# Kernel tuning notes

Measured on AMD Instinct MI355X. Metric: run time of the kernel, lower is better.

The kernel has to match this reference:

```python
import jax, jax.numpy as jnp
import numpy as np

NUM_CLASSES = 80
NUM_ATTRIB = 85
SCORE_THR = 0.05
CONF_THR = 0.005
IOU_THR = 0.45
MAX_DET = 100
PRE_NMS_TOPK = 4096  # top-k pre-filter; greedy NMS over these candidates


def _make_anchors():
    strides = [32, 16, 8]
    base_sizes = [[(116, 90), (156, 198), (373, 326)],
                  [(30, 61), (62, 45), (59, 119)],
                  [(10, 13), (16, 30), (33, 23)]]
    feat_sizes = [(19, 19), (38, 38), (76, 76)]
    anchors, strs = [], []
    for s, bs, (fh, fw) in zip(strides, base_sizes, feat_sizes):
        c = s / 2.0
        base = np.array([[c - 0.5 * w, c - 0.5 * h, c + 0.5 * w, c + 0.5 * h]
                         for (w, h) in bs], np.float32)
        xx = np.tile(np.arange(fw, dtype=np.float32) * s, fh)
        yy = np.repeat(np.arange(fh, dtype=np.float32) * s, fw)
        shifts = np.stack([xx, yy, xx, yy], -1)  # [HW,4]
        a = (shifts[:, None, :] + base[None, :, :]).reshape(-1, 4)  # location-major, anchor-minor
        anchors.append(a)
        strs.append(np.full(a.shape[0], s, np.float32))
    return np.concatenate(anchors), np.concatenate(strs)

_ANCHORS, _STRIDES = _make_anchors()


def _iou_one_to_many(box, boxes):
    tl = jnp.maximum(box[:2], boxes[:, :2])
    br = jnp.minimum(box[2:], boxes[:, 2:])
    inter = jnp.prod(jnp.clip(br - tl, 0.0), axis=-1)
    a1 = jnp.prod(box[2:] - box[:2])
    a2 = jnp.prod(boxes[:, 2:] - boxes[:, :2], axis=-1)
    return inter / (a1 + a2 - inter + 1e-12)


def _per_image(pred):  # pred: [N, 85]
    anchors = jnp.asarray(_ANCHORS)
    strides = jnp.asarray(_STRIDES)
    xy = jax.nn.sigmoid(pred[:, :2])
    obj = jax.nn.sigmoid(pred[:, 4])
    cls = jax.nn.sigmoid(pred[:, 5:])
    # decode_bboxes
    centers = (anchors[:, :2] + anchors[:, 2:]) * 0.5 + (xy - 0.5) * strides[:, None]
    whs = (anchors[:, 2:] - anchors[:, :2]) * 0.5 * jnp.exp(pred[:, 2:4])
    boxes = jnp.concatenate([centers - whs, centers + whs], axis=-1)  # [N,4]
    # conf threshold on objectness + score threshold on raw class score (torch order),
    # then multiply by objectness score factor
    valid = (obj[:, None] >= CONF_THR) & (cls > SCORE_THR)
    scores = jnp.where(valid, cls * obj[:, None], -jnp.inf).reshape(-1)  # [N*C]
    top_s, top_i = jax.lax.top_k(scores, PRE_NMS_TOPK)
    bidx = top_i // NUM_CLASSES
    labels = (top_i % NUM_CLASSES).astype(jnp.int32)
    cboxes = boxes[bidx]  # [K,4]
    finite = jnp.isfinite(top_s)
    max_coord = jnp.max(jnp.where(finite[:, None], cboxes, 0.0))
    off = labels.astype(boxes.dtype) * (max_coord + 1.0)  # per-class offset trick
    nms_boxes = cboxes + off[:, None]

    def body(i, state):
        alive, dets, det_labels = state
        j = jnp.argmax(alive)
        s = alive[j]
        keep = s > 0.0
        det = jnp.where(keep, jnp.concatenate([cboxes[j], s[None]]), 0.0)
        dets = dets.at[i].set(det)
        det_labels = det_labels.at[i].set(jnp.where(keep, labels[j], -1))
        suppress = _iou_one_to_many(nms_boxes[j], nms_boxes) > IOU_THR
        alive = jnp.where(suppress, -jnp.inf, alive).at[j].set(-jnp.inf)
        return alive, dets, det_labels

    dets0 = jnp.zeros((MAX_DET, 5), boxes.dtype)
    lbl0 = jnp.full((MAX_DET,), -1, jnp.int32)
    _, dets, det_labels = jax.lax.fori_loop(0, MAX_DET, body, (top_s, dets0, lbl0))
    return dets, det_labels


def _forward(pred_maps):
    B = pred_maps[0].shape[0]
    flat = [p.transpose(0, 2, 3, 1).reshape(B, -1, NUM_ATTRIB) for p in pred_maps]
    preds = jnp.concatenate(flat, axis=1)  # [B, N, 85]
    return jax.vmap(_per_image)(preds)  # dets [B,100,5], labels [B,100]


def setup_inputs() -> dict:
    key = jax.random.key(0)
    k0, k1, k2 = jax.random.split(key, 3)
    return {
        "pred_map0": jax.random.normal(k0, (16, 255, 19, 19), jnp.float32),
        "pred_map1": jax.random.normal(k1, (16, 255, 38, 38), jnp.float32),
        "pred_map2": jax.random.normal(k2, (16, 255, 76, 76), jnp.float32),
    }


def reference(pred_map0, pred_map1, pred_map2):
    return _forward([pred_map0, pred_map1, pred_map2])
```

## Files before the change

kernel.cpp:

```cpp
#include <hip/hip_runtime.h>
#include <stdint.h>
#include <math.h>

typedef unsigned long long u64;

#define CONF_THR   0.005f
#define SCORE_THRf 0.05f
#define IOU_THR    0.45f
#define TOPK       4096
#define MAXDET     100
#define NHIST      8192
#define NIMG       16
#define BCAP       8192
#define NSLICE     27
#define NBLK       (NIMG * NSLICE)
#define LCAP       1024

__constant__ float c_half[3][3][2] = {
  {{58.0f, 45.0f}, {78.0f, 99.0f}, {186.5f, 163.0f}},
  {{15.0f, 30.5f}, {31.0f, 22.5f}, {29.5f, 59.5f}},
  {{5.0f, 6.5f},  {8.0f, 15.0f},  {16.5f, 11.5f}},
};

__device__ __forceinline__ float sigmoidf_(float x) {
  return 1.0f / (1.0f + expf(-x));
}

__device__ __forceinline__ bool slice4_decode(const float* __restrict__ p0,
                                              const float* __restrict__ p1,
                                              const float* __restrict__ p2,
                                              int bx, int tid,
                                              int& b, const float*& q, int& HW,
                                              int& nstart, int& a, int& hw0, int& mi) {
  b = bx / NSLICE;
  int r = bx % NSLICE;
  int h0;
  if (r < 18)      { mi = 2; a = r / 6;         h0 = (r % 6) * 1024; }
  else if (r < 24) { mi = 1; a = (r - 18) >> 1; h0 = ((r - 18) & 1) * 1024; }
  else             { mi = 0; a = r - 24;        h0 = 0; }
  const float* p;
  if (mi == 2)      { p = p2; HW = 5776; nstart = 5415; }
  else if (mi == 1) { p = p1; HW = 1444; nstart = 1083; }
  else              { p = p0; HW = 361;  nstart = 0; }
  hw0 = h0 + tid * 4;
  if (hw0 >= HW) return false;
  q = p + (size_t)b * 255 * HW;
  return true;
}

template <bool PRIV>
__global__ void __launch_bounds__(256) k_hist(const float* __restrict__ p0,
                                              const float* __restrict__ p1,
                                              const float* __restrict__ p2,
                                              unsigned* __restrict__ outHist) {
  __shared__ unsigned lh[NHIST];
  for (int i = threadIdx.x; i < NHIST; i += 256) lh[i] = 0;
  __syncthreads();
  int b; const float* q; int HW, nstart, a, hw0, mi;
  bool act = slice4_decode(p0, p1, p2, blockIdx.x, threadIdx.x, b, q, HW, nstart, a, hw0, mi);
  if (act) {
    const float* orow = q + (size_t)(a * 85 + 4) * HW;
    float so[4]; bool ov[4] = {false, false, false, false};
    if (mi != 0) {
      float4 o = *(const float4*)(orow + hw0);
      so[0] = sigmoidf_(o.x); so[1] = sigmoidf_(o.y);
      so[2] = sigmoidf_(o.z); so[3] = sigmoidf_(o.w);
      #pragma unroll
      for (int k = 0; k < 4; ++k) ov[k] = so[k] >= CONF_THR;
    } else {
      #pragma unroll
      for (int k = 0; k < 4; ++k)
        if (hw0 + k < HW) { so[k] = sigmoidf_(orow[hw0 + k]); ov[k] = so[k] >= CONF_THR; }
    }
    for (int c = 0; c < 80; ++c) {
      const float* crow = q + (size_t)(a * 85 + 5 + c) * HW;
      float cv[4];
      if (mi != 0) {
        float4 v = *(const float4*)(crow + hw0);
        cv[0] = v.x; cv[1] = v.y; cv[2] = v.z; cv[3] = v.w;
      } else {
        #pragma unroll
        for (int k = 0; k < 4; ++k) cv[k] = (hw0 + k < HW) ? crow[hw0 + k] : -100.0f;
      }
      #pragma unroll
      for (int k = 0; k < 4; ++k) {
        if (!ov[k]) continue;
        float cs = sigmoidf_(cv[k]);
        if (cs > SCORE_THRf)
          atomicAdd(&lh[__float_as_uint(__fmul_rn(cs, so[k])) >> 17], 1u);
      }
    }
  }
  __syncthreads();
  if (PRIV) {
    unsigned* dst = outHist + (size_t)blockIdx.x * NHIST;
    for (int i = threadIdx.x * 4; i < NHIST; i += 1024)
      *(uint4*)(dst + i) = *(const uint4*)(&lh[i]);
  } else {
    unsigned* dst = outHist + (size_t)(blockIdx.x / NSLICE) * NHIST;
    for (int i = threadIdx.x; i < NHIST; i += 256) if (lh[i]) atomicAdd(&dst[i], lh[i]);
  }
}

__global__ void __launch_bounds__(256) k_merge(const unsigned* __restrict__ priv,
                                               unsigned* __restrict__ merged) {
  const int b = blockIdx.y;
  const int u = blockIdx.x * 256 + threadIdx.x;
  const unsigned* base = priv + (size_t)b * NSLICE * NHIST + u;
  unsigned s = 0;
  #pragma unroll
  for (int sl = 0; sl < NSLICE; ++sl) s += base[(size_t)sl * NHIST];
  merged[(size_t)b * NHIST + u] = s;
}

__global__ void k_scan(const unsigned* __restrict__ hist, int* __restrict__ bb1) {
  __shared__ unsigned h[NHIST];
  __shared__ unsigned csum[256];
  const int b = blockIdx.x;
  const unsigned* gh = hist + (size_t)b * NHIST;
  for (int i = threadIdx.x; i < NHIST; i += 256) h[i] = gh[i];
  __syncthreads();
  unsigned s = 0;
  for (int j = 0; j < 32; ++j) s += h[threadIdx.x * 32 + j];
  csum[threadIdx.x] = s;
  __syncthreads();
  if (threadIdx.x == 0) {
    unsigned acc = 0; int found = -1;
    for (int c2 = 255; c2 >= 0; --c2) {
      if (acc + csum[c2] >= TOPK) {
        for (int k2 = c2 * 32 + 31; k2 >= c2 * 32; --k2) {
          if (acc + h[k2] >= TOPK) { found = k2; break; }
          acc += h[k2];
        }
        break;
      } else acc += csum[c2];
    }
    bb1[b] = found;
  }
}

__global__ void __launch_bounds__(256) k_collect(const float* __restrict__ p0,
                                                 const float* __restrict__ p1,
                                                 const float* __restrict__ p2,
                                                 const int* __restrict__ bb1v,
                                                 unsigned* __restrict__ candCount,
                                                 unsigned* __restrict__ bCount,
                                                 u64* __restrict__ candKeys,
                                                 u64* __restrict__ blist) {
  __shared__ u64 wbuf[LCAP];
  __shared__ u64 bbuf[LCAP];
  __shared__ unsigned cnt2[2];
  __shared__ unsigned base2[2];
  if (threadIdx.x < 2) cnt2[threadIdx.x] = 0;
  __syncthreads();
  int b; const float* q; int HW, nstart, a, hw0, mi;
  bool act = slice4_decode(p0, p1, p2, blockIdx.x, threadIdx.x, b, q, HW, nstart, a, hw0, mi);
  const int bglobal = blockIdx.x / NSLICE;
  const int Bb1 = bb1v[bglobal];
  u64* ckg = candKeys + (size_t)bglobal * TOPK;
  u64* blg = blist + (size_t)bglobal * BCAP;

  if (act) {
    const float T = (Bb1 > 0) ? __uint_as_float((unsigned)Bb1 << 17) : 0.0f;
    const float* orow = q + (size_t)(a * 85 + 4) * HW;
    float so[4]; bool ov[4] = {false, false, false, false};
    if (mi != 0) {
      float4 o = *(const float4*)(orow + hw0);
      so[0] = sigmoidf_(o.x); so[1] = sigmoidf_(o.y);
      so[2] = sigmoidf_(o.z); so[3] = sigmoidf_(o.w);
      #pragma unroll
      for (int k = 0; k < 4; ++k) ov[k] = so[k] >= CONF_THR;
    } else {
      #pragma unroll
      for (int k = 0; k < 4; ++k)
        if (hw0 + k < HW) { so[k] = sigmoidf_(orow[hw0 + k]); ov[k] = so[k] >= CONF_THR; }
    }
    float cth[4];
    #pragma unroll
    for (int k = 0; k < 4; ++k) {
      cth[k] = 1e30f;
      if (ov[k]) {
        cth[k] = -1e30f;
        if (Bb1 > 0) {
          float u = __fdiv_rn(T, so[k]);
          cth[k] = (u >= 1.0f) ? 15.0f : (logf(__fdiv_rn(u, __fsub_rn(1.0f, u))) - 0.05f);
        }
      }
    }
    for (int c = 0; c < 80; ++c) {
      const float* crow = q + (size_t)(a * 85 + 5 + c) * HW;
      float cv[4];
      if (mi != 0) {
        float4 v = *(const float4*)(crow + hw0);
        cv[0] = v.x; cv[1] = v.y; cv[2] = v.z; cv[3] = v.w;
      } else {
        #pragma unroll
        for (int k = 0; k < 4; ++k) cv[k] = (hw0 + k < HW) ? crow[hw0 + k] : -100.0f;
      }
      #pragma unroll
      for (int k = 0; k < 4; ++k) {
        if (cv[k] <= cth[k]) continue;
        float cs = sigmoidf_(cv[k]);
        if (cs <= SCORE_THRf) continue;
        unsigned bits = __float_as_uint(__fmul_rn(cs, so[k]));
        int bkt = (int)(bits >> 17);
        if (bkt < Bb1) continue;
        unsigned idx = (unsigned)((nstart + (hw0 + k) * 3 + a) * 80 + c);
        u64 key = ((u64)(bits ^ 0x80000000u) << 32) | (u64)(0xFFFFFFFFu - idx);
        if (bkt > Bb1) {
          unsigned pos = atomicAdd(&cnt2[0], 1u);
          if (pos < LCAP) wbuf[pos] = key;
          else { unsigned g = atomicAdd(&candCount[bglobal], 1u); if (g < TOPK) ckg[g] = key; }
        } else {
          unsigned pos = atomicAdd(&cnt2[1], 1u);
          if (pos < LCAP) bbuf[pos] = key;
          else { unsigned g = atomicAdd(&bCount[bglobal], 1u); if (g < BCAP) blg[g] = key; }
        }
      }
    }
  }
  __syncthreads();
  unsigned wn = min(cnt2[0], (unsigned)LCAP);
  unsigned bn = min(cnt2[1], (unsigned)LCAP);
  if (threadIdx.x == 0) base2[0] = wn ? atomicAdd(&candCount[bglobal], wn) : 0u;
  if (threadIdx.x == 1) base2[1] = bn ? atomicAdd(&bCount[bglobal], bn) : 0u;
  __syncthreads();
  for (unsigned i = threadIdx.x; i < wn; i += 256) {
    unsigned g = base2[0] + i; if (g < TOPK) ckg[g] = wbuf[i];
  }
  for (unsigned i = threadIdx.x; i < bn; i += 256) {
    unsigned g = base2[1] + i; if (g < BCAP) blg[g] = bbuf[i];
  }
}

__device__ __forceinline__ int swz(int i) { return i ^ ((i >> 4) & 0xF); }

__device__ __forceinline__ u64 shflx64(u64 x, int m) {
  unsigned lo = __shfl_xor((unsigned)x, m);
  unsigned hi = __shfl_xor((unsigned)(x >> 32), m);
  return ((u64)hi << 32) | lo;
}

template <int V>
__device__ void bitonic_hybrid_desc(u64* sb, u64 (&r)[V], int t) {
  const int N = 1024 * V;
  for (int k = 2; k <= N; k <<= 1) {
    for (int j = k >> 1; j > 0; j >>= 1) {
      if (j >= 64 * V) {
        __syncthreads();
        #pragma unroll
        for (int v = 0; v < V; ++v) sb[swz(t * V + v)] = r[v];
        __syncthreads();
        #pragma unroll
        for (int v = 0; v < V; ++v) {
          int i = t * V + v;
          u64 A = r[v], B = sb[swz(i ^ j)];
          bool up = (i & k) == 0, lower = (i & j) == 0;
          r[v] = (up == lower) ? (A > B ? A : B) : (A < B ? A : B);
        }
      } else if (j >= V) {
        int d = j / V;
        #pragma unroll
        for (int v = 0; v < V; ++v) {
          int i = t * V + v;
          u64 A = r[v], B = shflx64(r[v], d);
          bool up = (i & k) == 0, lower = (i & j) == 0;
          r[v] = (up == lower) ? (A > B ? A : B) : (A < B ? A : B);
        }
      } else {
        #pragma unroll
        for (int v = 0; v < V; ++v) {
          if ((v & j) == 0) {
            int i = t * V + v;
            u64 A = r[v], B = r[v ^ j];
            bool up = (i & k) == 0;
            u64 mx = A > B ? A : B, mn = A > B ? B : A;
            r[v] = up ? mx : mn; r[v ^ j] = up ? mn : mx;
          }
        }
      }
    }
  }
}

__global__ void __launch_bounds__(1024) k_sortdecode(
    const unsigned* __restrict__ candCount, const unsigned* __restrict__ bCount,
    u64* __restrict__ candKeys, const u64* __restrict__ blist,
    const float* __restrict__ p0, const float* __restrict__ p1, const float* __restrict__ p2,
    float4* __restrict__ boxS, float* __restrict__ maxcv) {
  __shared__ u64 sb[8192];
  const int b = blockIdx.x, t = threadIdx.x;
  unsigned C1 = candCount[b]; if (C1 > TOPK) C1 = TOPK;
  unsigned m = bCount[b];     if (m > BCAP) m = BCAP;
  int need = TOPK - (int)C1;
  int take = need > 0 ? (need < (int)m ? need : (int)m) : 0;
  const u64* bl = blist + (size_t)b * BCAP;
  u64* ck = candKeys + (size_t)b * TOPK;
  if (take > 0) {
    u64 r8[8];
    #pragma unroll
    for (int v = 0; v < 8; ++v) { int i = t * 8 + v; r8[v] = (i < (int)m) ? bl[i] : 0ull; }
    bitonic_hybrid_desc<8>(sb, r8, t);
    __syncthreads();
    #pragma unroll
    for (int v = 0; v < 8; ++v) sb[swz(t * 8 + v)] = r8[v];
  }
  __syncthreads();
  u64 r4[4];
  #pragma unroll
  for (int v = 0; v < 4; ++v) {
    int i = t * 4 + v;
    u64 key = 0ull;
    if (i < (int)C1) key = ck[i];
    else if (i < (int)C1 + take) key = sb[swz(i - (int)C1)];
    r4[v] = key;
  }
  __syncthreads();
  bitonic_hybrid_desc<4>(sb, r4, t);
  float lmax = -INFINITY;
  float4* bs = boxS + (size_t)b * TOPK;
  #pragma unroll
  for (int v = 0; v < 4; ++v) {
    int i = t * 4 + v;
    u64 key = r4[v];
    ck[i] = key;
    float4 bx = make_float4(0.f, 0.f, 0.f, 0.f);
    float contrib = 0.0f;
    if (key != 0ull) {
      unsigned idx = 0xFFFFFFFFu - (unsigned)(key & 0xFFFFFFFFull);
      int n = (int)(idx / 80u);
      const float* p; int HW, W, nstart, L; float fs;
      if (n < 1083)      { p = p0; HW = 361;  W = 19; nstart = 0;    fs = 32.f; L = 0; }
      else if (n < 5415) { p = p1; HW = 1444; W = 38; nstart = 1083; fs = 16.f; L = 1; }
      else               { p = p2; HW = 5776; W = 76; nstart = 5415; fs = 8.f;  L = 2; }
      int r = n - nstart; int hw = r / 3; int an = r % 3;
      int gx = hw % W;    int gy = hw / W;
      const float* qq = p + (size_t)b * 255 * HW + hw;
      float tx = qq[(size_t)(an * 85 + 0) * HW];
      float ty = qq[(size_t)(an * 85 + 1) * HW];
      float tw = qq[(size_t)(an * 85 + 2) * HW];
      float th = qq[(size_t)(an * 85 + 3) * HW];
      float acx = __fadd_rn((float)gx * fs, 0.5f * fs);
      float acy = __fadd_rn((float)gy * fs, 0.5f * fs);
      float sx = sigmoidf_(tx), sy = sigmoidf_(ty);
      float cx = __fadd_rn(acx, __fmul_rn(__fsub_rn(sx, 0.5f), fs));
      float cy = __fadd_rn(acy, __fmul_rn(__fsub_rn(sy, 0.5f), fs));
      float wx = __fmul_rn(c_half[L][an][0], expf(tw));
      float wy = __fmul_rn(c_half[L][an][1], expf(th));
      bx.x = __fsub_rn(cx, wx); bx.y = __fsub_rn(cy, wy);
      bx.z = __fadd_rn(cx, wx); bx.w = __fadd_rn(cy, wy);
      contrib = fmaxf(fmaxf(bx.x, bx.y), fmaxf(bx.z, bx.w));
    }
    bs[i] = bx;
    lmax = fmaxf(lmax, contrib);
  }
  float* red = (float*)(sb + 4096);
  red[t] = lmax;
  for (int s = 512; s > 0; s >>= 1) {
    __syncthreads();
    if (t < s) red[t] = fmaxf(red[t], red[t + s]);
  }
  __syncthreads();
  if (t == 0) maxcv[b] = red[0];
}

__global__ void __launch_bounds__(64) k_nms(const u64* __restrict__ candKeys,
                                            const float4* __restrict__ boxS,
                                            const float* __restrict__ maxcv,
                                            float* __restrict__ out) {
  const int b = blockIdx.x;
  const int lane = threadIdx.x;
  float* dets = out + (size_t)b * (MAXDET * 5);
  float* lbls = out + (size_t)NIMG * MAXDET * 5 + (size_t)b * MAXDET;
  for (int i = lane; i < MAXDET; i += 64) {
    dets[i * 5 + 0] = 0.f; dets[i * 5 + 1] = 0.f; dets[i * 5 + 2] = 0.f;
    dets[i * 5 + 3] = 0.f; dets[i * 5 + 4] = 0.f;
    lbls[i] = -1.0f;
  }
  const float mc1 = __fadd_rn(maxcv[b], 1.0f);
  const u64* ck = candKeys + (size_t)b * TOPK;
  const float4* bs = boxS + (size_t)b * TOPK;
  float pbx1[2], pby1[2], pbx2[2], pby2[2], parea[2];
  int P = 0;
  bool done = false;
  for (int base = 0; base < TOPK && !done; base += 64) {
    const int e = base + lane;
    u64 key = ck[e];
    float score = -INFINITY; int c = 0;
    float4 bx = bs[e];
    if (key) {
      unsigned mb = (unsigned)(key >> 32);
      score = __uint_as_float(mb ^ 0x80000000u);
      unsigned idx = 0xFFFFFFFFu - (unsigned)(key & 0xFFFFFFFFull);
      c = (int)(idx % 80u);
    }
    float off = __fmul_rn((float)c, mc1);
    float nx1 = __fadd_rn(bx.x, off), ny1 = __fadd_rn(bx.y, off);
    float nx2 = __fadd_rn(bx.z, off), ny2 = __fadd_rn(bx.w, off);
    for (int tt = 0; tt < 64; ++tt) {
      float s_e = __shfl(score, tt);
      if (!(s_e > 0.0f)) { done = true; break; }
      float ex1 = __shfl(nx1, tt), ey1 = __shfl(ny1, tt);
      float ex2 = __shfl(nx2, tt), ey2 = __shfl(ny2, tt);
      float ea = __fmul_rn(__fsub_rn(ex2, ex1), __fsub_rn(ey2, ey1));
      bool sup = false;
      #pragma unroll
      for (int k2 = 0; k2 < 2; ++k2) {
        int pi = k2 * 64 + lane;
        if (pi < P) {
          float tlx = fmaxf(pbx1[k2], ex1), tly = fmaxf(pby1[k2], ey1);
          float brx = fminf(pbx2[k2], ex2), bry = fminf(pby2[k2], ey2);
          float iw = fmaxf(__fsub_rn(brx, tlx), 0.0f);
          float ih = fmaxf(__fsub_rn(bry, tly), 0.0f);
          float inter = __fmul_rn(iw, ih);
          float denom = __fadd_rn(__fsub_rn(__fadd_rn(parea[k2], ea), inter), 1e-12f);
          float iou = __fdiv_rn(inter, denom);
          if (iou > IOU_THR) sup = true;
        }
      }
      if (!__any(sup)) {
        float cx1 = __shfl(bx.x, tt), cy1 = __shfl(bx.y, tt);
        float cx2 = __shfl(bx.z, tt), cy2 = __shfl(bx.w, tt);
        int   ce  = __shfl(c, tt);
        if (lane == (P & 63)) {
          int slot = P >> 6;
          pbx1[slot] = ex1; pby1[slot] = ey1; pbx2[slot] = ex2; pby2[slot] = ey2;
          parea[slot] = ea;
        }
        if (lane == 0) {
          dets[P * 5 + 0] = cx1; dets[P * 5 + 1] = cy1;
          dets[P * 5 + 2] = cx2; dets[P * 5 + 3] = cy2;
          dets[P * 5 + 4] = s_e;
          lbls[P] = (float)ce;
        }
        ++P;
        if (P == MAXDET) { done = true; break; }
      }
    }
  }
}

extern "C" void kernel_launch(void* const* d_in, const int* in_sizes, int n_in,
                              void* d_out, int out_size, void* d_ws, size_t ws_size,
                              hipStream_t stream) {
  const float* p0 = (const float*)d_in[0];
  const float* p1 = (const float*)d_in[1];
  const float* p2 = (const float*)d_in[2];
  float* out = (float*)d_out;
  char* ws = (char*)d_ws;

  const size_t OFF_MERGED = 0;
  const size_t OFF_CNT    = 524288;
  const size_t OFF_CK     = 524544;
  const size_t OFF_BL     = 1048832;
  const size_t OFF_BOX    = 2097408;
  const size_t OFF_PRIV   = 3145984;
  const size_t NEED_PRIV  = OFF_PRIV + (size_t)NBLK * NHIST * 4;

  unsigned* merged = (unsigned*)(ws + OFF_MERGED);
  unsigned* candCount = (unsigned*)(ws + OFF_CNT);
  unsigned* bCount = candCount + 16;
  int* bb1 = (int*)(bCount + 16);
  float* maxcv = (float*)(bb1 + 16);
  u64* candKeys = (u64*)(ws + OFF_CK);
  u64* blist = (u64*)(ws + OFF_BL);
  float4* boxS = (float4*)(ws + OFF_BOX);
  unsigned* priv = (unsigned*)(ws + OFF_PRIV);

  const bool use_priv = ws_size >= NEED_PRIV;
  if (use_priv) {
    hipMemsetAsync(ws + OFF_CNT, 0, 256, stream);
    k_hist<true><<<NBLK, 256, 0, stream>>>(p0, p1, p2, priv);
    k_merge<<<dim3(NHIST / 256, NIMG), 256, 0, stream>>>(priv, merged);
  } else {
    hipMemsetAsync(ws, 0, OFF_CNT + 256, stream);
    k_hist<false><<<NBLK, 256, 0, stream>>>(p0, p1, p2, merged);
  }
  k_scan<<<NIMG, 256, 0, stream>>>(merged, bb1);
  k_collect<<<NBLK, 256, 0, stream>>>(p0, p1, p2, bb1, candCount, bCount, candKeys, blist);
  k_sortdecode<<<NIMG, 1024, 0, stream>>>(candCount, bCount, candKeys, blist,
                                          p0, p1, p2, boxS, maxcv);
  k_nms<<<NIMG, 64, 0, stream>>>(candKeys, boxS, maxcv, out);
}
```

Measured before the change: 461.2 us.

## Split sort into boundary-select, per-chunk sorts, and merge; finer histogram slicing

The single per-image sort+decode kernel (16 blocks) is split into three kernels. A boundary-bucket select sorts only the needed boundary candidates, 64 blocks each sort a 1024-key chunk with the correct bitonic direction offset, and a final kernel runs only the last two merge stages before decoding boxes. The histogram kernel also moves to 48 slices of 128 threads per image to raise block-level parallelism over the input reads. The cost is extra kernel launches and global round-trips of the candidate keys, plus a plain LDS bitonic sort for the boundary list.

```diff
diff --git a/kernel.cpp b/kernel.cpp
--- a/kernel.cpp
+++ b/kernel.cpp
@@ -12,9 +12,11 @@
 #define NHIST      8192
 #define NIMG       16
 #define BCAP       8192
-#define NSLICE     27
-#define NBLK       (NIMG * NSLICE)
 #define LCAP       1024
+#define NSLICE_C   27
+#define NBLK_C     (NIMG * NSLICE_C)
+#define NSLICE_H   48
+#define NBLK_H     (NIMG * NSLICE_H)
 
 __constant__ float c_half[3][3][2] = {
   {{58.0f, 45.0f}, {78.0f, 99.0f}, {186.5f, 163.0f}},
@@ -26,14 +28,14 @@
   return 1.0f / (1.0f + expf(-x));
 }
 
-__device__ __forceinline__ bool slice4_decode(const float* __restrict__ p0,
-                                              const float* __restrict__ p1,
-                                              const float* __restrict__ p2,
-                                              int bx, int tid,
-                                              int& b, const float*& q, int& HW,
-                                              int& nstart, int& a, int& hw0, int& mi) {
-  b = bx / NSLICE;
-  int r = bx % NSLICE;
+__device__ __forceinline__ bool slice_c(const float* __restrict__ p0,
+                                        const float* __restrict__ p1,
+                                        const float* __restrict__ p2,
+                                        int bx, int tid,
+                                        int& b, const float*& q, int& HW,
+                                        int& nstart, int& a, int& hw0, int& mi) {
+  b = bx / NSLICE_C;
+  int r = bx % NSLICE_C;
   int h0;
   if (r < 18)      { mi = 2; a = r / 6;         h0 = (r % 6) * 1024; }
   else if (r < 24) { mi = 1; a = (r - 18) >> 1; h0 = ((r - 18) & 1) * 1024; }
@@ -48,16 +50,38 @@
   return true;
 }
 
+__device__ __forceinline__ bool slice_h(const float* __restrict__ p0,
+                                        const float* __restrict__ p1,
+                                        const float* __restrict__ p2,
+                                        int bx, int tid,
+                                        int& b, const float*& q, int& HW,
+                                        int& a, int& hw0, int& mi) {
+  b = bx / NSLICE_H;
+  int r = bx % NSLICE_H;
+  int ch;
+  if (r < 36)      { mi = 2; a = r / 12;       ch = r % 12; }
+  else if (r < 45) { mi = 1; a = (r - 36) / 3; ch = (r - 36) % 3; }
+  else             { mi = 0; a = r - 45;       ch = 0; }
+  const float* p;
+  if (mi == 2)      { p = p2; HW = 5776; }
+  else if (mi == 1) { p = p1; HW = 1444; }
+  else              { p = p0; HW = 361; }
+  hw0 = ch * 512 + tid * 4;
+  if (hw0 >= HW) return false;
+  q = p + (size_t)b * 255 * HW;
+  return true;
+}
+
 template <bool PRIV>
-__global__ void __launch_bounds__(256) k_hist(const float* __restrict__ p0,
+__global__ void __launch_bounds__(128) k_hist(const float* __restrict__ p0,
                                               const float* __restrict__ p1,
                                               const float* __restrict__ p2,
                                               unsigned* __restrict__ outHist) {
   __shared__ unsigned lh[NHIST];
-  for (int i = threadIdx.x; i < NHIST; i += 256) lh[i] = 0;
-  __syncthreads();
-  int b; const float* q; int HW, nstart, a, hw0, mi;
-  bool act = slice4_decode(p0, p1, p2, blockIdx.x, threadIdx.x, b, q, HW, nstart, a, hw0, mi);
+  for (int i = threadIdx.x; i < NHIST; i += 128) lh[i] = 0;
+  __syncthreads();
+  int b; const float* q; int HW, a, hw0, mi;
+  bool act = slice_h(p0, p1, p2, blockIdx.x, threadIdx.x, b, q, HW, a, hw0, mi);
   if (act) {
     const float* orow = q + (size_t)(a * 85 + 4) * HW;
     float so[4]; bool ov[4] = {false, false, false, false};
@@ -94,11 +118,11 @@
   __syncthreads();
   if (PRIV) {
     unsigned* dst = outHist + (size_t)blockIdx.x * NHIST;
-    for (int i = threadIdx.x * 4; i < NHIST; i += 1024)
+    for (int i = threadIdx.x * 4; i < NHIST; i += 512)
       *(uint4*)(dst + i) = *(const uint4*)(&lh[i]);
   } else {
-    unsigned* dst = outHist + (size_t)(blockIdx.x / NSLICE) * NHIST;
-    for (int i = threadIdx.x; i < NHIST; i += 256) if (lh[i]) atomicAdd(&dst[i], lh[i]);
+    unsigned* dst = outHist + (size_t)(blockIdx.x / NSLICE_H) * NHIST;
+    for (int i = threadIdx.x; i < NHIST; i += 128) if (lh[i]) atomicAdd(&dst[i], lh[i]);
   }
 }
 
@@ -106,10 +130,10 @@
                                                unsigned* __restrict__ merged) {
   const int b = blockIdx.y;
   const int u = blockIdx.x * 256 + threadIdx.x;
-  const unsigned* base = priv + (size_t)b * NSLICE * NHIST + u;
+  const unsigned* base = priv + (size_t)b * NSLICE_H * NHIST + u;
   unsigned s = 0;
   #pragma unroll
-  for (int sl = 0; sl < NSLICE; ++sl) s += base[(size_t)sl * NHIST];
+  for (int sl = 0; sl < NSLICE_H; ++sl) s += base[(size_t)sl * NHIST];
   merged[(size_t)b * NHIST + u] = s;
 }
 
@@ -154,8 +178,8 @@
   if (threadIdx.x < 2) cnt2[threadIdx.x] = 0;
   __syncthreads();
   int b; const float* q; int HW, nstart, a, hw0, mi;
-  bool act = slice4_decode(p0, p1, p2, blockIdx.x, threadIdx.x, b, q, HW, nstart, a, hw0, mi);
-  const int bglobal = blockIdx.x / NSLICE;
+  bool act = slice_c(p0, p1, p2, blockIdx.x, threadIdx.x, b, q, HW, nstart, a, hw0, mi);
+  const int bglobal = blockIdx.x / NSLICE_C;
   const int Bb1 = bb1v[bglobal];
   u64* ckg = candKeys + (size_t)bglobal * TOPK;
   u64* blg = blist + (size_t)bglobal * BCAP;
@@ -241,10 +265,25 @@
   return ((u64)hi << 32) | lo;
 }
 
-template <int V>
-__device__ void bitonic_hybrid_desc(u64* sb, u64 (&r)[V], int t) {
-  const int N = 1024 * V;
-  for (int k = 2; k <= N; k <<= 1) {
+__device__ void bitonic_lds_desc(u64* sb, int p2, int nthr, int t) {
+  for (int k = 2; k <= p2; k <<= 1) {
+    for (int j = k >> 1; j > 0; j >>= 1) {
+      for (int i = t; i < p2; i += nthr) {
+        int ixj = i ^ j;
+        if (ixj > i) {
+          u64 A = sb[swz(i)], B = sb[swz(ixj)];
+          bool up = (i & k) == 0;
+          if (up ? (A < B) : (A > B)) { sb[swz(i)] = B; sb[swz(ixj)] = A; }
+        }
+      }
+      __syncthreads();
+    }
+  }
+}
+
+template <int V, int NTHR>
+__device__ void bitonic_stages(u64* sb, u64 (&r)[V], int t, int kFrom, int kTo, int iofs) {
+  for (int k = kFrom; k <= kTo; k <<= 1) {
     for (int j = k >> 1; j > 0; j >>= 1) {
       if (j >= 64 * V) {
         __syncthreads();
@@ -255,7 +294,7 @@
         for (int v = 0; v < V; ++v) {
           int i = t * V + v;
           u64 A = r[v], B = sb[swz(i ^ j)];
-          bool up = (i & k) == 0, lower = (i & j) == 0;
+          bool up = ((i + iofs) & k) == 0, lower = (i & j) == 0;
           r[v] = (up == lower) ? (A > B ? A : B) : (A < B ? A : B);
         }
       } else if (j >= V) {
@@ -264,7 +303,7 @@
         for (int v = 0; v < V; ++v) {
           int i = t * V + v;
           u64 A = r[v], B = shflx64(r[v], d);
-          bool up = (i & k) == 0, lower = (i & j) == 0;
+          bool up = ((i + iofs) & k) == 0, lower = (i & j) == 0;
           r[v] = (up == lower) ? (A > B ? A : B) : (A < B ? A : B);
         }
       } else {
@@ -273,7 +312,7 @@
           if ((v & j) == 0) {
             int i = t * V + v;
             u64 A = r[v], B = r[v ^ j];
-            bool up = (i & k) == 0;
+            bool up = ((i + iofs) & k) == 0;
             u64 mx = A > B ? A : B, mn = A > B ? B : A;
             r[v] = up ? mx : mn; r[v ^ j] = up ? mn : mx;
           }
@@ -283,46 +322,58 @@
   }
 }
 
-__global__ void __launch_bounds__(1024) k_sortdecode(
-    const unsigned* __restrict__ candCount, const unsigned* __restrict__ bCount,
-    u64* __restrict__ candKeys, const u64* __restrict__ blist,
-    const float* __restrict__ p0, const float* __restrict__ p1, const float* __restrict__ p2,
-    float4* __restrict__ boxS, float* __restrict__ maxcv) {
-  __shared__ u64 sb[8192];
+__global__ void __launch_bounds__(1024) k_bsel(const unsigned* __restrict__ candCount,
+                                               const unsigned* __restrict__ bCount,
+                                               u64* __restrict__ candKeys,
+                                               const u64* __restrict__ blist) {
+  __shared__ u64 sb[BCAP];
   const int b = blockIdx.x, t = threadIdx.x;
   unsigned C1 = candCount[b]; if (C1 > TOPK) C1 = TOPK;
   unsigned m = bCount[b];     if (m > BCAP) m = BCAP;
   int need = TOPK - (int)C1;
   int take = need > 0 ? (need < (int)m ? need : (int)m) : 0;
+  u64* ck = candKeys + (size_t)b * TOPK;
   const u64* bl = blist + (size_t)b * BCAP;
+  if (take > 0) {
+    int p2 = 1; while (p2 < (int)m) p2 <<= 1;
+    for (int i = t; i < p2; i += 1024) sb[swz(i)] = (i < (int)m) ? bl[i] : 0ull;
+    __syncthreads();
+    bitonic_lds_desc(sb, p2, 1024, t);
+    for (int i = t; i < take; i += 1024) ck[C1 + i] = sb[swz(i)];
+  }
+  for (int i = (int)C1 + take + t; i < TOPK; i += 1024) ck[i] = 0ull;
+}
+
+__global__ void __launch_bounds__(256) k_chunksort(u64* __restrict__ candKeys) {
+  __shared__ u64 sb[1024];
+  const int img = blockIdx.x >> 2, c = blockIdx.x & 3, t = threadIdx.x;
+  u64* ck = candKeys + (size_t)img * TOPK + c * 1024;
+  u64 r[4];
+  #pragma unroll
+  for (int v = 0; v < 4; ++v) r[v] = ck[t * 4 + v];
+  bitonic_stages<4, 256>(sb, r, t, 2, 1024, c * 1024);
+  #pragma unroll
+  for (int v = 0; v < 4; ++v) ck[t * 4 + v] = r[v];
+}
+
+__global__ void __launch_bounds__(1024) k_mergedecode(
+    u64* __restrict__ candKeys,
+    const float* __restrict__ p0, const float* __restrict__ p1, const float* __restrict__ p2,
+    float4* __restrict__ boxS, float* __restrict__ maxcv) {
+  __shared__ u64 sb[TOPK];
+  __shared__ float red[1024];
+  const int b = blockIdx.x, t = threadIdx.x;
   u64* ck = candKeys + (size_t)b * TOPK;
-  if (take > 0) {
-    u64 r8[8];
-    #pragma unroll
-    for (int v = 0; v < 8; ++v) { int i = t * 8 + v; r8[v] = (i < (int)m) ? bl[i] : 0ull; }
-    bitonic_hybrid_desc<8>(sb, r8, t);
-    __syncthreads();
-    #pragma unroll
-    for (int v = 0; v < 8; ++v) sb[swz(t * 8 + v)] = r8[v];
-  }
-  __syncthreads();
-  u64 r4[4];
+  u64 r[4];
   #pragma unroll
-  for (int v = 0; v < 4; ++v) {
-    int i = t * 4 + v;
-    u64 key = 0ull;
-    if (i < (int)C1) key = ck[i];
-    else if (i < (int)C1 + take) key = sb[swz(i - (int)C1)];
-    r4[v] = key;
-  }
-  __syncthreads();
-  bitonic_hybrid_desc<4>(sb, r4, t);
+  for (int v = 0; v < 4; ++v) r[v] = ck[t * 4 + v];
+  bitonic_stages<4, 1024>(sb, r, t, 2048, 4096, 0);
   float lmax = -INFINITY;
   float4* bs = boxS + (size_t)b * TOPK;
   #pragma unroll
   for (int v = 0; v < 4; ++v) {
     int i = t * 4 + v;
-    u64 key = r4[v];
+    u64 key = r[v];
     ck[i] = key;
     float4 bx = make_float4(0.f, 0.f, 0.f, 0.f);
     float contrib = 0.0f;
@@ -333,8 +384,8 @@
       if (n < 1083)      { p = p0; HW = 361;  W = 19; nstart = 0;    fs = 32.f; L = 0; }
       else if (n < 5415) { p = p1; HW = 1444; W = 38; nstart = 1083; fs = 16.f; L = 1; }
       else               { p = p2; HW = 5776; W = 76; nstart = 5415; fs = 8.f;  L = 2; }
-      int r = n - nstart; int hw = r / 3; int an = r % 3;
-      int gx = hw % W;    int gy = hw / W;
+      int rr = n - nstart; int hw = rr / 3; int an = rr % 3;
+      int gx = hw % W;     int gy = hw / W;
       const float* qq = p + (size_t)b * 255 * HW + hw;
       float tx = qq[(size_t)(an * 85 + 0) * HW];
       float ty = qq[(size_t)(an * 85 + 1) * HW];
@@ -354,7 +405,6 @@
     bs[i] = bx;
     lmax = fmaxf(lmax, contrib);
   }
-  float* red = (float*)(sb + 4096);
   red[t] = lmax;
   for (int s = 512; s > 0; s >>= 1) {
     __syncthreads();
@@ -455,7 +505,7 @@
   const size_t OFF_BL     = 1048832;
   const size_t OFF_BOX    = 2097408;
   const size_t OFF_PRIV   = 3145984;
-  const size_t NEED_PRIV  = OFF_PRIV + (size_t)NBLK * NHIST * 4;
+  const size_t NEED_PRIV  = OFF_PRIV + (size_t)NBLK_H * NHIST * 4;
 
   unsigned* merged = (unsigned*)(ws + OFF_MERGED);
   unsigned* candCount = (unsigned*)(ws + OFF_CNT);
@@ -470,15 +520,16 @@
   const bool use_priv = ws_size >= NEED_PRIV;
   if (use_priv) {
     hipMemsetAsync(ws + OFF_CNT, 0, 256, stream);
-    k_hist<true><<<NBLK, 256, 0, stream>>>(p0, p1, p2, priv);
+    k_hist<true><<<NBLK_H, 128, 0, stream>>>(p0, p1, p2, priv);
     k_merge<<<dim3(NHIST / 256, NIMG), 256, 0, stream>>>(priv, merged);
   } else {
     hipMemsetAsync(ws, 0, OFF_CNT + 256, stream);
-    k_hist<false><<<NBLK, 256, 0, stream>>>(p0, p1, p2, merged);
+    k_hist<false><<<NBLK_H, 128, 0, stream>>>(p0, p1, p2, merged);
   }
   k_scan<<<NIMG, 256, 0, stream>>>(merged, bb1);
-  k_collect<<<NBLK, 256, 0, stream>>>(p0, p1, p2, bb1, candCount, bCount, candKeys, blist);
-  k_sortdecode<<<NIMG, 1024, 0, stream>>>(candCount, bCount, candKeys, blist,
-                                          p0, p1, p2, boxS, maxcv);
+  k_collect<<<NBLK_C, 256, 0, stream>>>(p0, p1, p2, bb1, candCount, bCount, candKeys, blist);
+  k_bsel<<<NIMG, 1024, 0, stream>>>(candCount, bCount, candKeys, blist);
+  k_chunksort<<<NIMG * 4, 256, 0, stream>>>(candKeys);
+  k_mergedecode<<<NIMG, 1024, 0, stream>>>(candKeys, p0, p1, p2, boxS, maxcv);
   k_nms<<<NIMG, 64, 0, stream>>>(candKeys, boxS, maxcv, out);
 }
```

New measurement: 396.1 us. -14.1%, faster.
